# Optimization experiments

Hardware: AMD Instinct MI355X
Metric: run time of the kernel (lower is better)

The kernel has to match this reference:

```python
import jax, jax.numpy as jnp
import numpy as np

N = 100000      # nodes
E = 1600000     # edges
G = 256         # graphs in the batch
D_IN = 128
H = 128
C = 10
EPS = 1e-5      # BatchNorm eps


def setup_inputs() -> dict:
    key = jax.random.key(0)
    ks = jax.random.split(key, 32)
    inp = {
        'x': jax.random.normal(ks[0], (N, D_IN), jnp.float32),
        'edge_index': jax.random.randint(ks[1], (2, E), 0, N, dtype=jnp.int64),
        'batch': jnp.sort(jax.random.randint(ks[2], (N,), 0, G, dtype=jnp.int64)),
        'w1': jax.random.normal(ks[3], (D_IN, H), jnp.float32) * 0.05,
        'b1': jax.random.normal(ks[4], (H,), jnp.float32) * 0.05,
        'w2': jax.random.normal(ks[5], (H, H), jnp.float32) * 0.05,
        'b2': jax.random.normal(ks[6], (H,), jnp.float32) * 0.05,
        'w3': jax.random.normal(ks[7], (H, H), jnp.float32) * 0.05,
        'b3': jax.random.normal(ks[8], (H,), jnp.float32) * 0.05,
        'g1': jax.random.uniform(ks[9], (H,), jnp.float32, 0.5, 1.5),
        'be1': jax.random.normal(ks[10], (H,), jnp.float32) * 0.05,
        'm1': jax.random.normal(ks[11], (H,), jnp.float32) * 0.05,
        'v1': jax.random.uniform(ks[12], (H,), jnp.float32, 0.5, 1.5),
        'g2': jax.random.uniform(ks[13], (H,), jnp.float32, 0.5, 1.5),
        'be2': jax.random.normal(ks[14], (H,), jnp.float32) * 0.05,
        'm2': jax.random.normal(ks[15], (H,), jnp.float32) * 0.05,
        'v2': jax.random.uniform(ks[16], (H,), jnp.float32, 0.5, 1.5),
        'g3': jax.random.uniform(ks[17], (H,), jnp.float32, 0.5, 1.5),
        'be3': jax.random.normal(ks[18], (H,), jnp.float32) * 0.05,
        'm3': jax.random.normal(ks[19], (H,), jnp.float32) * 0.05,
        'v3': jax.random.uniform(ks[20], (H,), jnp.float32, 0.5, 1.5),
        'fcw1': jax.random.normal(ks[21], (H, H // 2), jnp.float32) * 0.05,
        'fcb1': jax.random.normal(ks[22], (H // 2,), jnp.float32) * 0.05,
        'fcw2': jax.random.normal(ks[23], (H // 2, C), jnp.float32) * 0.05,
        'fcb2': jax.random.normal(ks[24], (C,), jnp.float32) * 0.05,
    }
    return inp


def _gcn_norm(edge_index, n_nodes):
    # add self loops (PyG GCNConv default) and compute D^-1/2 (A+I) D^-1/2 norms
    loop = jnp.arange(n_nodes, dtype=edge_index.dtype)
    src = jnp.concatenate([edge_index[0], loop])
    dst = jnp.concatenate([edge_index[1], loop])
    deg = jax.ops.segment_sum(jnp.ones_like(dst, dtype=jnp.float32), dst, num_segments=n_nodes)
    dinv = jnp.where(deg > 0, jax.lax.rsqrt(deg), 0.0)
    norm = dinv[src] * dinv[dst]  # [E+N]
    return src, dst, norm


def _gcn_conv(x, W, b, src, dst, norm, n_nodes):
    h = x @ W                                   # [N, H]
    msg = norm[:, None] * h[src]                # gather + scale, [E+N, H]
    return jax.ops.segment_sum(msg, dst, num_segments=n_nodes) + b


def _bn_eval(x, gamma, beta, mean, var):
    return (x - mean) * jax.lax.rsqrt(var + EPS) * gamma + beta


def reference(x, edge_index, batch, w1, b1, w2, b2, w3, b3,
              g1, be1, m1, v1, g2, be2, m2, v2, g3, be3, m3, v3,
              fcw1, fcb1, fcw2, fcb2):
    n = x.shape[0]
    x = jnp.nan_to_num(x, nan=0.0, posinf=1e6, neginf=-1e6)
    src, dst, norm = _gcn_norm(edge_index, n)

    h = jax.nn.relu(_bn_eval(_gcn_conv(x, w1, b1, src, dst, norm, n), g1, be1, m1, v1))
    h = jax.nn.relu(_bn_eval(_gcn_conv(h, w2, b2, src, dst, norm, n), g2, be2, m2, v2))
    h = jax.nn.relu(_bn_eval(_gcn_conv(h, w3, b3, src, dst, norm, n), g3, be3, m3, v3))

    # global_mean_pool over graphs
    sums = jax.ops.segment_sum(h, batch, num_segments=G)            # [G, H]
    cnts = jax.ops.segment_sum(jnp.ones((n,), h.dtype), batch, num_segments=G)
    pooled = sums / jnp.maximum(cnts, 1.0)[:, None]

    out = jax.nn.relu(pooled @ fcw1 + fcb1) @ fcw2 + fcb2           # [G, C]
    return out
```

## Files before the change

### kernel.cpp

```cpp
#include <hip/hip_runtime.h>
#include <math.h>

#define NN 100000
#define EE 1600000
#define GG 256
#define HH 128
#define BSH 8
#define NBK 391
#define PASSA_WG 391
#define CAPB 5120

typedef __attribute__((ext_vector_type(8))) short short8;
typedef __attribute__((ext_vector_type(4))) float f32x4;

union U4S8 { uint4 u; short8 s; };

static __device__ __forceinline__ unsigned bf16rne(float f) {
    const unsigned u = __float_as_uint(f);
    return (u + 0x7fffu + ((u >> 16) & 1u)) >> 16;
}
static __device__ __forceinline__ unsigned packbf(float a, float b) {
    return bf16rne(a) | (bf16rne(b) << 16);
}
static __device__ __forceinline__ float bflo(unsigned u) { return __uint_as_float(u << 16); }
static __device__ __forceinline__ float bfhi(unsigned u) { return __uint_as_float(u & 0xffff0000u); }

__global__ void detect_k(const int* __restrict__ ei, const int* __restrict__ batch,
                         int* __restrict__ flags) {
    if (threadIdx.x == 0 && blockIdx.x == 0) {
        int e64 = 1;
        for (int j = 0; j < 8; ++j) {
            if (ei[2 * EE - 1 - 2 * j] != 0) { e64 = 0; break; }
        }
        flags[0] = e64;
        flags[1] = (batch[NN - 1] == 0) ? 1 : 0;
    }
}

__global__ __launch_bounds__(512) void cursinit_k(int* __restrict__ cursor) {
    const int b = blockIdx.x * 512 + threadIdx.x;
    if (b < NBK) cursor[b] = b * CAPB;
}

__global__ void bnprep_k(const float* __restrict__ b1, const float* __restrict__ g1,
                         const float* __restrict__ be1, const float* __restrict__ m1,
                         const float* __restrict__ v1,
                         const float* __restrict__ b2, const float* __restrict__ g2,
                         const float* __restrict__ be2, const float* __restrict__ m2,
                         const float* __restrict__ v2,
                         const float* __restrict__ b3, const float* __restrict__ g3,
                         const float* __restrict__ be3, const float* __restrict__ m3,
                         const float* __restrict__ v3,
                         float* __restrict__ sc, float* __restrict__ sh) {
    const int c = threadIdx.x;
    float s;
    s = g1[c] / sqrtf(v1[c] + 1e-5f);
    sc[c] = s;           sh[c] = (b1[c] - m1[c]) * s + be1[c];
    s = g2[c] / sqrtf(v2[c] + 1e-5f);
    sc[128 + c] = s;     sh[128 + c] = (b2[c] - m2[c]) * s + be2[c];
    s = g3[c] / sqrtf(v3[c] + 1e-5f);
    sc[256 + c] = s;     sh[256 + c] = (b3[c] - m3[c]) * s + be3[c];
}

__global__ __launch_bounds__(256) void wprep_k(const float* __restrict__ w1,
                                               const float* __restrict__ w2,
                                               const float* __restrict__ w3,
                                               unsigned* __restrict__ bt) {
    const int id = blockIdx.x * 256 + threadIdx.x;
    if (id >= 3 * 8192) return;
    const int w = id >> 13;
    const int rem = id & 8191;
    const int n = rem >> 6;
    const int kk = rem & 63;
    const float* W = (w == 0) ? w1 : (w == 1) ? w2 : w3;
    bt[id] = packbf(W[(2 * kk) * HH + n], W[(2 * kk + 1) * HH + n]);
}

__global__ __launch_bounds__(256) void passA_k(const int* __restrict__ ei,
                                               const int* __restrict__ flags,
                                               int* __restrict__ cursor,
                                               unsigned* __restrict__ pairs) {
    __shared__ int h[NBK];
    __shared__ int rbase[NBK];
    const int tid = threadIdx.x;
    for (int i = tid; i < NBK; i += 256) h[i] = 0;
    __syncthreads();
    const bool e64 = flags[0] != 0;
    const int base = blockIdx.x * 4096;
    int scache[16], dcache[16];
#pragma unroll
    for (int j = 0; j < 16; ++j) {
        const int e = base + j * 256 + tid;
        int s = -1, d = 0;
        if (e < EE) {
            s = e64 ? ei[2 * e] : ei[e];
            d = e64 ? ei[2 * (EE + e)] : ei[EE + e];
            atomicAdd(&h[d >> BSH], 1);
        }
        scache[j] = s; dcache[j] = d;
    }
    __syncthreads();
    for (int i = tid; i < NBK; i += 256) {
        const int c = h[i];
        rbase[i] = c ? atomicAdd(&cursor[i], c) : 0;
    }
    __syncthreads();
    for (int i = tid; i < NBK; i += 256) h[i] = 0;
    __syncthreads();
#pragma unroll
    for (int j = 0; j < 16; ++j) {
        const int s = scache[j];
        if (s >= 0) {
            const int d = dcache[j];
            const int b = d >> BSH;
            const int r = atomicAdd(&h[b], 1);
            pairs[rbase[b] + r] = ((unsigned)(d & 255) << 17) | (unsigned)s;
        }
    }
}

__global__ __launch_bounds__(256) void passB_k(const unsigned* __restrict__ pairs,
                                               const int* __restrict__ cursor,
                                               int* __restrict__ offs,
                                               int* __restrict__ degcnt,
                                               float* __restrict__ dinv,
                                               int* __restrict__ csr) {
    __shared__ unsigned pk[CAPB];
    __shared__ int cnt[256];
    __shared__ int loff[256];
    __shared__ int sc[256];
    const int tid = threadIdx.x;
    const int b = blockIdx.x;
    const int p0 = b * CAPB;
    const int np = cursor[b] - p0;
    const int nb0 = b << BSH;
    const int nnode = (NN - nb0 < 256) ? (NN - nb0) : 256;

    cnt[tid] = 0;
    __syncthreads();
    for (int i = tid; i < np; i += 256) {
        const unsigned p = pairs[p0 + i];
        pk[i] = p;
        atomicAdd(&cnt[p >> 17], 1);
    }
    __syncthreads();
    sc[tid] = cnt[tid];
    __syncthreads();
    for (int off = 1; off < 256; off <<= 1) {
        int t = (tid >= off) ? sc[tid - off] : 0;
        __syncthreads();
        sc[tid] += t;
        __syncthreads();
    }
    const int ex = sc[tid] - cnt[tid];
    loff[tid] = ex;
    if (tid < nnode) {
        const int node = nb0 + tid;
        offs[node] = p0 + ex;
        degcnt[node] = cnt[tid];
        dinv[node] = 1.0f / sqrtf((float)(cnt[tid] + 1));
    }
    __syncthreads();
    cnt[tid] = 0;
    __syncthreads();
    for (int i = tid; i < np; i += 256) {
        const unsigned p = pk[i];
        const int dl = (int)(p >> 17);
        const int r = atomicAdd(&cnt[dl], 1);
        csr[p0 + loff[dl] + r] = (int)(p & 0x1FFFFu);
    }
}

static __device__ __forceinline__ float sani(float v) {
    if (isnan(v)) return 0.0f;
    if (isinf(v)) return v > 0.0f ? 1e6f : -1e6f;
    return v;
}

template <bool AF32>
__global__ __launch_bounds__(256) void gemm_mfma_k(const float* __restrict__ Af,
                                                   const unsigned* __restrict__ Abf,
                                                   const unsigned* __restrict__ btg,
                                                   unsigned* __restrict__ C, int M) {
    __shared__ unsigned lds_u[8704];
    const int tid = threadIdx.x;
    const int wave = tid >> 6;
    const int lane = tid & 63;
    const int nl = lane & 15;
    const int q = lane >> 4;

    {
        const uint4* __restrict__ bg4 = (const uint4*)btg;
        for (int i = tid; i < 2048; i += 256) {
            const int n = i >> 4, w4 = i & 15;
            *(uint4*)&lds_u[n * 68 + w4 * 4] = bg4[n * 16 + w4];
        }
    }
    __syncthreads();

    const int row0 = blockIdx.x * 64 + wave * 16;
    const int rowa = min(row0 + nl, M - 1);

    short8 a[4];
    if (AF32) {
#pragma unroll
        for (int ks = 0; ks < 4; ++ks) {
            const float4 p = *(const float4*)(Af + (size_t)rowa * HH + ks * 32 + q * 8);
            const float4 r = *(const float4*)(Af + (size_t)rowa * HH + ks * 32 + q * 8 + 4);
            U4S8 cv;
            cv.u = make_uint4(packbf(sani(p.x), sani(p.y)), packbf(sani(p.z), sani(p.w)),
                              packbf(sani(r.x), sani(r.y)), packbf(sani(r.z), sani(r.w)));
            a[ks] = cv.s;
        }
    } else {
#pragma unroll
        for (int ks = 0; ks < 4; ++ks) {
            U4S8 cv;
            cv.u = *(const uint4*)(Abf + (size_t)rowa * 64 + ks * 16 + q * 4);
            a[ks] = cv.s;
        }
    }

    f32x4 acc[8];
#pragma unroll
    for (int t = 0; t < 8; ++t) acc[t] = (f32x4)0.0f;

    const unsigned short* __restrict__ bts = (const unsigned short*)lds_u;
#pragma unroll
    for (int ks = 0; ks < 4; ++ks) {
#pragma unroll
        for (int t = 0; t < 8; ++t) {
            const int n = t * 16 + nl;
            const short8 b = *(const short8*)(bts + n * 136 + ks * 32 + q * 8);
            acc[t] = __builtin_amdgcn_mfma_f32_16x16x32_bf16(a[ks], b, acc[t], 0, 0, 0);
        }
    }

    __syncthreads();

    float* __restrict__ cs = (float*)lds_u + wave * 16 * 132;
#pragma unroll
    for (int t = 0; t < 8; ++t) {
#pragma unroll
        for (int r = 0; r < 4; ++r) {
            cs[(q * 4 + r) * 132 + t * 16 + nl] = acc[t][r];
        }
    }
    __syncthreads();

    const int rr = lane & 15;
    const int seg = lane >> 4;
    const int rowg = row0 + rr;
    if (rowg < M) {
        const float4* crow = (const float4*)(cs + rr * 132) + seg * 8;
#pragma unroll
        for (int j = 0; j < 4; ++j) {
            const float4 fa = crow[2 * j];
            const float4 fb = crow[2 * j + 1];
            const uint4 o = make_uint4(packbf(fa.x, fa.y), packbf(fa.z, fa.w),
                                       packbf(fb.x, fb.y), packbf(fb.z, fb.w));
            *(uint4*)(C + (size_t)rowg * 64 + seg * 16 + j * 4) = o;
        }
    }
}

__global__ __launch_bounds__(256) void aggregate_k(
    const unsigned* __restrict__ hpre, const int* __restrict__ csr,
    const int* __restrict__ offs, const int* __restrict__ cnt,
    const float* __restrict__ dinv,
    const float* __restrict__ bnsc, const float* __restrict__ bnsh,
    unsigned* __restrict__ xout) {
    const int v = __builtin_amdgcn_readfirstlane(blockIdx.x * 4 + (threadIdx.x >> 6));
    const int lane = threadIdx.x & 63;
    const int cg = lane & 15;
    const int sub = lane >> 4;
    const int c8 = cg * 8;

    const float dv = dinv[v];
    const int start = offs[v];
    const int n = cnt[v];
    const char* __restrict__ hb = (const char*)hpre;
    const unsigned cgo = (unsigned)(cg << 4);

    float acc[8];
#pragma unroll
    for (int j = 0; j < 8; ++j) acc[j] = 0.0f;

    for (int i = 0; i < n; i += 16) {
        const int e0 = i + sub, e1 = i + 4 + sub, e2 = i + 8 + sub, e3 = i + 12 + sub;
        const int nm1 = n - 1;
        const int s0 = csr[start + min(e0, nm1)];
        const int s1 = csr[start + min(e1, nm1)];
        const int s2 = csr[start + min(e2, nm1)];
        const int s3 = csr[start + min(e3, nm1)];
        const float w0 = (e0 < n) ? dinv[s0] : 0.0f;
        const float w1 = (e1 < n) ? dinv[s1] : 0.0f;
        const float w2 = (e2 < n) ? dinv[s2] : 0.0f;
        const float w3 = (e3 < n) ? dinv[s3] : 0.0f;
        const uint4 r0 = *(const uint4*)(hb + (((unsigned)s0 << 8) | cgo));
        const uint4 r1 = *(const uint4*)(hb + (((unsigned)s1 << 8) | cgo));
        const uint4 r2 = *(const uint4*)(hb + (((unsigned)s2 << 8) | cgo));
        const uint4 r3 = *(const uint4*)(hb + (((unsigned)s3 << 8) | cgo));

        acc[0] += w0 * bflo(r0.x); acc[1] += w0 * bfhi(r0.x);
        acc[2] += w0 * bflo(r0.y); acc[3] += w0 * bfhi(r0.y);
        acc[4] += w0 * bflo(r0.z); acc[5] += w0 * bfhi(r0.z);
        acc[6] += w0 * bflo(r0.w); acc[7] += w0 * bfhi(r0.w);
        acc[0] += w1 * bflo(r1.x); acc[1] += w1 * bfhi(r1.x);
        acc[2] += w1 * bflo(r1.y); acc[3] += w1 * bfhi(r1.y);
        acc[4] += w1 * bflo(r1.z); acc[5] += w1 * bfhi(r1.z);
        acc[6] += w1 * bflo(r1.w); acc[7] += w1 * bfhi(r1.w);
        acc[0] += w2 * bflo(r2.x); acc[1] += w2 * bfhi(r2.x);
        acc[2] += w2 * bflo(r2.y); acc[3] += w2 * bfhi(r2.y);
        acc[4] += w2 * bflo(r2.z); acc[5] += w2 * bfhi(r2.z);
        acc[6] += w2 * bflo(r2.w); acc[7] += w2 * bfhi(r2.w);
        acc[0] += w3 * bflo(r3.x); acc[1] += w3 * bfhi(r3.x);
        acc[2] += w3 * bflo(r3.y); acc[3] += w3 * bfhi(r3.y);
        acc[4] += w3 * bflo(r3.z); acc[5] += w3 * bfhi(r3.z);
        acc[6] += w3 * bflo(r3.w); acc[7] += w3 * bfhi(r3.w);
    }

#pragma unroll
    for (int j = 0; j < 8; ++j) {
        acc[j] += __shfl_xor(acc[j], 16);
        acc[j] += __shfl_xor(acc[j], 32);
    }

    if (sub == 0) {
        const float4 sca = *(const float4*)(bnsc + c8);
        const float4 scb = *(const float4*)(bnsc + c8 + 4);
        const float4 sha = *(const float4*)(bnsh + c8);
        const float4 shb = *(const float4*)(bnsh + c8 + 4);
        const uint4 rs = *(const uint4*)(hb + (((unsigned)v << 8) | cgo));
        const float dv2 = dv * dv;
        const float s0 = dv * acc[0] + dv2 * bflo(rs.x);
        const float s1 = dv * acc[1] + dv2 * bfhi(rs.x);
        const float s2 = dv * acc[2] + dv2 * bflo(rs.y);
        const float s3 = dv * acc[3] + dv2 * bfhi(rs.y);
        const float s4 = dv * acc[4] + dv2 * bflo(rs.z);
        const float s5 = dv * acc[5] + dv2 * bfhi(rs.z);
        const float s6 = dv * acc[6] + dv2 * bflo(rs.w);
        const float s7 = dv * acc[7] + dv2 * bfhi(rs.w);
        const float y0 = fmaxf(s0 * sca.x + sha.x, 0.0f);
        const float y1 = fmaxf(s1 * sca.y + sha.y, 0.0f);
        const float y2 = fmaxf(s2 * sca.z + sha.z, 0.0f);
        const float y3 = fmaxf(s3 * sca.w + sha.w, 0.0f);
        const float y4 = fmaxf(s4 * scb.x + shb.x, 0.0f);
        const float y5 = fmaxf(s5 * scb.y + shb.y, 0.0f);
        const float y6 = fmaxf(s6 * scb.z + shb.z, 0.0f);
        const float y7 = fmaxf(s7 * scb.w + shb.w, 0.0f);
        *(uint4*)(xout + (size_t)v * 64 + cg * 4) =
            make_uint4(packbf(y0, y1), packbf(y2, y3), packbf(y4, y5), packbf(y6, y7));
    }
}

__global__ __launch_bounds__(256) void pool_sum_k(
    const unsigned* __restrict__ x, const int* __restrict__ batch,
    const int* __restrict__ flags, float* __restrict__ psum,
    int* __restrict__ gcnt) {
    const int wave = threadIdx.x >> 6;
    const int lane = threadIdx.x & 63;
    const int row0 = blockIdx.x * 64 + wave * 16;
    if (row0 >= NN) return;
    const bool b64 = flags[1] != 0;

    float sx = 0.0f, sy = 0.0f;
    int cur = -1, runlen = 0;
#pragma unroll
    for (int r = 0; r < 16; ++r) {
        const int row = row0 + r;
        if (row >= NN) break;
        const int g = b64 ? batch[2 * row] : batch[row];
        if (g != cur) {
            if (cur >= 0) {
                atomicAdd(&psum[cur * HH + lane * 2 + 0], sx);
                atomicAdd(&psum[cur * HH + lane * 2 + 1], sy);
                if (lane == 0) atomicAdd(&gcnt[cur], runlen);
            }
            cur = g; sx = 0.0f; sy = 0.0f; runlen = 0;
        }
        const unsigned u = x[(size_t)row * 64 + lane];
        sx += bflo(u);
        sy += bfhi(u);
        ++runlen;
    }
    if (cur >= 0) {
        atomicAdd(&psum[cur * HH + lane * 2 + 0], sx);
        atomicAdd(&psum[cur * HH + lane * 2 + 1], sy);
        if (lane == 0) atomicAdd(&gcnt[cur], runlen);
    }
}

__global__ __launch_bounds__(128) void head_k(
    const float* __restrict__ psum, const int* __restrict__ gcnt,
    const float* __restrict__ fw1, const float* __restrict__ fb1,
    const float* __restrict__ fw2, const float* __restrict__ fb2,
    float* __restrict__ out) {
    __shared__ float pooled[128];
    __shared__ float hid[64];
    const int g = blockIdx.x;
    const int tid = threadIdx.x;

    const int cntn = gcnt[g];
    pooled[tid] = psum[g * HH + tid] / (float)(cntn > 0 ? cntn : 1);
    __syncthreads();

    if (tid < 64) {
        float a = fb1[tid];
#pragma unroll 4
        for (int k = 0; k < 128; ++k) a += pooled[k] * fw1[k * 64 + tid];
        hid[tid] = fmaxf(a, 0.0f);
    }
    __syncthreads();
    if (tid < 10) {
        float a = fb2[tid];
#pragma unroll
        for (int k = 0; k < 64; ++k) a += hid[k] * fw2[k * 10 + tid];
        out[g * 10 + tid] = a;
    }
}

extern "C" void kernel_launch(void* const* d_in, const int* in_sizes, int n_in,
                              void* d_out, int out_size, void* d_ws, size_t ws_size,
                              hipStream_t stream) {
    const float* x_in  = (const float*)d_in[0];
    const int*   ei    = (const int*)d_in[1];
    const int*   batch = (const int*)d_in[2];
    const float* w1 = (const float*)d_in[3];
    const float* b1 = (const float*)d_in[4];
    const float* w2 = (const float*)d_in[5];
    const float* b2 = (const float*)d_in[6];
    const float* w3 = (const float*)d_in[7];
    const float* b3 = (const float*)d_in[8];
    const float* g1 = (const float*)d_in[9];
    const float* be1 = (const float*)d_in[10];
    const float* m1 = (const float*)d_in[11];
    const float* v1 = (const float*)d_in[12];
    const float* g2 = (const float*)d_in[13];
    const float* be2 = (const float*)d_in[14];
    const float* m2 = (const float*)d_in[15];
    const float* v2 = (const float*)d_in[16];
    const float* g3 = (const float*)d_in[17];
    const float* be3 = (const float*)d_in[18];
    const float* m3 = (const float*)d_in[19];
    const float* v3 = (const float*)d_in[20];
    const float* fw1 = (const float*)d_in[21];
    const float* fb1 = (const float*)d_in[22];
    const float* fw2 = (const float*)d_in[23];
    const float* fb2 = (const float*)d_in[24];
    float* out = (float*)d_out;

    size_t off = 0;
    char* base = (char*)d_ws;
    auto alloc = [&](size_t bytes) -> void* {
        void* p = base + off;
        off += (bytes + 255) & ~(size_t)255;
        return p;
    };
    int*      degcnt = (int*)alloc((size_t)NN * 4);
    float*    dinv   = (float*)alloc((size_t)NN * 4);
    int*      offs   = (int*)alloc((size_t)NN * 4);
    int*      cursor = (int*)alloc((size_t)NBK * 4);
    int*      flags  = (int*)alloc(256);
    float*    bnsc   = (float*)alloc(3 * 128 * 4);
    float*    bnsh   = (float*)alloc(3 * 128 * 4);
    unsigned* btg    = (unsigned*)alloc(3 * 8192 * 4);
    float*    psum   = (float*)alloc((size_t)GG * HH * 4);
    int*      gcnt   = (int*)alloc((size_t)GG * 4);
    int*      csr    = (int*)alloc((size_t)NBK * CAPB * 4);
    unsigned* pairs  = (unsigned*)alloc((size_t)NBK * CAPB * 4);
    unsigned* bufx   = (unsigned*)alloc((size_t)NN * 64 * 4);
    unsigned* hpre   = (unsigned*)alloc((size_t)NN * 64 * 4);
    if (off > ws_size) return;

    detect_k<<<1, 64, 0, stream>>>(ei, batch, flags);
    cursinit_k<<<1, 512, 0, stream>>>(cursor);
    bnprep_k<<<1, 128, 0, stream>>>(b1, g1, be1, m1, v1,
                                    b2, g2, be2, m2, v2,
                                    b3, g3, be3, m3, v3, bnsc, bnsh);
    wprep_k<<<96, 256, 0, stream>>>(w1, w2, w3, btg);
    hipMemsetAsync(psum, 0, (size_t)GG * HH * 4, stream);
    hipMemsetAsync(gcnt, 0, (size_t)GG * 4, stream);
    passA_k<<<PASSA_WG, 256, 0, stream>>>(ei, flags, cursor, pairs);
    passB_k<<<NBK, 256, 0, stream>>>(pairs, cursor, offs, degcnt, dinv, csr);

    const int ggrid = (NN + 63) / 64;
    const int agrid = NN / 4;

    gemm_mfma_k<true><<<ggrid, 256, 0, stream>>>(x_in, nullptr, btg, hpre, NN);
    aggregate_k<<<agrid, 256, 0, stream>>>(hpre, csr, offs, degcnt, dinv,
                                           bnsc, bnsh, bufx);
    gemm_mfma_k<false><<<ggrid, 256, 0, stream>>>(nullptr, bufx, btg + 8192, hpre, NN);
    aggregate_k<<<agrid, 256, 0, stream>>>(hpre, csr, offs, degcnt, dinv,
                                           bnsc + 128, bnsh + 128, bufx);
    gemm_mfma_k<false><<<ggrid, 256, 0, stream>>>(nullptr, bufx, btg + 16384, hpre, NN);
    aggregate_k<<<agrid, 256, 0, stream>>>(hpre, csr, offs, degcnt, dinv,
                                           bnsc + 256, bnsh + 256, bufx);

    pool_sum_k<<<ggrid, 256, 0, stream>>>(bufx, batch, flags, psum, gcnt);
    head_k<<<GG, 128, 0, stream>>>(psum, gcnt, fw1, fb1, fw2, fb2, out);
}
```

Baseline: 470.1 us.

## Prescale GEMM output by source dinv and pad CSR rows with self-loop and zero row

```diff
diff --git a/kernel.cpp b/kernel.cpp
--- a/kernel.cpp
+++ b/kernel.cpp
@@ -8,7 +8,7 @@
 #define BSH 8
 #define NBK 391
 #define PASSA_WG 391
-#define CAPB 5120
+#define CAPB 5632
 
 typedef __attribute__((ext_vector_type(8))) short short8;
 typedef __attribute__((ext_vector_type(4))) float f32x4;
@@ -144,7 +144,9 @@
         atomicAdd(&cnt[p >> 17], 1);
     }
     __syncthreads();
-    sc[tid] = cnt[tid];
+    const int creal = cnt[tid];
+    const int cpad = (tid < nnode) ? ((creal + 4) & ~3) : 0;
+    sc[tid] = cpad;
     __syncthreads();
     for (int off = 1; off < 256; off <<= 1) {
         int t = (tid >= off) ? sc[tid - off] : 0;
@@ -152,13 +154,13 @@
         sc[tid] += t;
         __syncthreads();
     }
-    const int ex = sc[tid] - cnt[tid];
+    const int ex = sc[tid] - cpad;
     loff[tid] = ex;
     if (tid < nnode) {
         const int node = nb0 + tid;
         offs[node] = p0 + ex;
-        degcnt[node] = cnt[tid];
-        dinv[node] = 1.0f / sqrtf((float)(cnt[tid] + 1));
+        degcnt[node] = creal;
+        dinv[node] = 1.0f / sqrtf((float)(creal + 1));
     }
     __syncthreads();
     cnt[tid] = 0;
@@ -169,6 +171,11 @@
         const int r = atomicAdd(&cnt[dl], 1);
         csr[p0 + loff[dl] + r] = (int)(p & 0x1FFFFu);
     }
+    if (tid < nnode) {
+        const int basep = p0 + loff[tid];
+        csr[basep + creal] = nb0 + tid;
+        for (int j = creal + 1; j < cpad; ++j) csr[basep + j] = NN;
+    }
 }
 
 static __device__ __forceinline__ float sani(float v) {
@@ -181,6 +188,7 @@
 __global__ __launch_bounds__(256) void gemm_mfma_k(const float* __restrict__ Af,
                                                    const unsigned* __restrict__ Abf,
                                                    const unsigned* __restrict__ btg,
+                                                   const float* __restrict__ dinv,
                                                    unsigned* __restrict__ C, int M) {
     __shared__ unsigned lds_u[8704];
     const int tid = threadIdx.x;
@@ -252,15 +260,23 @@
     const int seg = lane >> 4;
     const int rowg = row0 + rr;
     if (rowg < M) {
+        const float dsc = dinv[rowg];
         const float4* crow = (const float4*)(cs + rr * 132) + seg * 8;
 #pragma unroll
         for (int j = 0; j < 4; ++j) {
             const float4 fa = crow[2 * j];
             const float4 fb = crow[2 * j + 1];
-            const uint4 o = make_uint4(packbf(fa.x, fa.y), packbf(fa.z, fa.w),
-                                       packbf(fb.x, fb.y), packbf(fb.z, fb.w));
+            const uint4 o = make_uint4(packbf(dsc * fa.x, dsc * fa.y),
+                                       packbf(dsc * fa.z, dsc * fa.w),
+                                       packbf(dsc * fb.x, dsc * fb.y),
+                                       packbf(dsc * fb.z, dsc * fb.w));
             *(uint4*)(C + (size_t)rowg * 64 + seg * 16 + j * 4) = o;
         }
+    } else if (rowg == M) {
+        const uint4 z = make_uint4(0, 0, 0, 0);
+#pragma unroll
+        for (int j = 0; j < 4; ++j)
+            *(uint4*)(C + (size_t)M * 64 + seg * 16 + j * 4) = z;
     }
 }
 
@@ -278,7 +294,7 @@
 
     const float dv = dinv[v];
     const int start = offs[v];
-    const int n = cnt[v];
+    const int npad = (cnt[v] + 4) & ~3;
     const char* __restrict__ hb = (const char*)hpre;
     const unsigned cgo = (unsigned)(cg << 4);
 
@@ -286,38 +302,28 @@
 #pragma unroll
     for (int j = 0; j < 8; ++j) acc[j] = 0.0f;
 
-    for (int i = 0; i < n; i += 16) {
-        const int e0 = i + sub, e1 = i + 4 + sub, e2 = i + 8 + sub, e3 = i + 12 + sub;
-        const int nm1 = n - 1;
-        const int s0 = csr[start + min(e0, nm1)];
-        const int s1 = csr[start + min(e1, nm1)];
-        const int s2 = csr[start + min(e2, nm1)];
-        const int s3 = csr[start + min(e3, nm1)];
-        const float w0 = (e0 < n) ? dinv[s0] : 0.0f;
-        const float w1 = (e1 < n) ? dinv[s1] : 0.0f;
-        const float w2 = (e2 < n) ? dinv[s2] : 0.0f;
-        const float w3 = (e3 < n) ? dinv[s3] : 0.0f;
-        const uint4 r0 = *(const uint4*)(hb + (((unsigned)s0 << 8) | cgo));
-        const uint4 r1 = *(const uint4*)(hb + (((unsigned)s1 << 8) | cgo));
-        const uint4 r2 = *(const uint4*)(hb + (((unsigned)s2 << 8) | cgo));
-        const uint4 r3 = *(const uint4*)(hb + (((unsigned)s3 << 8) | cgo));
-
-        acc[0] += w0 * bflo(r0.x); acc[1] += w0 * bfhi(r0.x);
-        acc[2] += w0 * bflo(r0.y); acc[3] += w0 * bfhi(r0.y);
-        acc[4] += w0 * bflo(r0.z); acc[5] += w0 * bfhi(r0.z);
-        acc[6] += w0 * bflo(r0.w); acc[7] += w0 * bfhi(r0.w);
-        acc[0] += w1 * bflo(r1.x); acc[1] += w1 * bfhi(r1.x);
-        acc[2] += w1 * bflo(r1.y); acc[3] += w1 * bfhi(r1.y);
-        acc[4] += w1 * bflo(r1.z); acc[5] += w1 * bfhi(r1.z);
-        acc[6] += w1 * bflo(r1.w); acc[7] += w1 * bfhi(r1.w);
-        acc[0] += w2 * bflo(r2.x); acc[1] += w2 * bfhi(r2.x);
-        acc[2] += w2 * bflo(r2.y); acc[3] += w2 * bfhi(r2.y);
-        acc[4] += w2 * bflo(r2.z); acc[5] += w2 * bfhi(r2.z);
-        acc[6] += w2 * bflo(r2.w); acc[7] += w2 * bfhi(r2.w);
-        acc[0] += w3 * bflo(r3.x); acc[1] += w3 * bfhi(r3.x);
-        acc[2] += w3 * bflo(r3.y); acc[3] += w3 * bfhi(r3.y);
-        acc[4] += w3 * bflo(r3.z); acc[5] += w3 * bfhi(r3.z);
-        acc[6] += w3 * bflo(r3.w); acc[7] += w3 * bfhi(r3.w);
+    int i = 0;
+    for (; i + 8 <= npad; i += 8) {
+        const int sA = csr[start + i + sub];
+        const int sB = csr[start + i + 4 + sub];
+        const uint4 rA = *(const uint4*)(hb + (((unsigned)sA << 8) | cgo));
+        const uint4 rB = *(const uint4*)(hb + (((unsigned)sB << 8) | cgo));
+        acc[0] += bflo(rA.x) + bflo(rB.x);
+        acc[1] += bfhi(rA.x) + bfhi(rB.x);
+        acc[2] += bflo(rA.y) + bflo(rB.y);
+        acc[3] += bfhi(rA.y) + bfhi(rB.y);
+        acc[4] += bflo(rA.z) + bflo(rB.z);
+        acc[5] += bfhi(rA.z) + bfhi(rB.z);
+        acc[6] += bflo(rA.w) + bflo(rB.w);
+        acc[7] += bfhi(rA.w) + bfhi(rB.w);
+    }
+    if (i < npad) {
+        const int s = csr[start + i + sub];
+        const uint4 r = *(const uint4*)(hb + (((unsigned)s << 8) | cgo));
+        acc[0] += bflo(r.x); acc[1] += bfhi(r.x);
+        acc[2] += bflo(r.y); acc[3] += bfhi(r.y);
+        acc[4] += bflo(r.z); acc[5] += bfhi(r.z);
+        acc[6] += bflo(r.w); acc[7] += bfhi(r.w);
     }
 
 #pragma unroll
@@ -331,24 +337,14 @@
         const float4 scb = *(const float4*)(bnsc + c8 + 4);
         const float4 sha = *(const float4*)(bnsh + c8);
         const float4 shb = *(const float4*)(bnsh + c8 + 4);
-        const uint4 rs = *(const uint4*)(hb + (((unsigned)v << 8) | cgo));
-        const float dv2 = dv * dv;
-        const float s0 = dv * acc[0] + dv2 * bflo(rs.x);
-        const float s1 = dv * acc[1] + dv2 * bfhi(rs.x);
-        const float s2 = dv * acc[2] + dv2 * bflo(rs.y);
-        const float s3 = dv * acc[3] + dv2 * bfhi(rs.y);
-        const float s4 = dv * acc[4] + dv2 * bflo(rs.z);
-        const float s5 = dv * acc[5] + dv2 * bfhi(rs.z);
-        const float s6 = dv * acc[6] + dv2 * bflo(rs.w);
-        const float s7 = dv * acc[7] + dv2 * bfhi(rs.w);
-        const float y0 = fmaxf(s0 * sca.x + sha.x, 0.0f);
-        const float y1 = fmaxf(s1 * sca.y + sha.y, 0.0f);
-        const float y2 = fmaxf(s2 * sca.z + sha.z, 0.0f);
-        const float y3 = fmaxf(s3 * sca.w + sha.w, 0.0f);
-        const float y4 = fmaxf(s4 * scb.x + shb.x, 0.0f);
-        const float y5 = fmaxf(s5 * scb.y + shb.y, 0.0f);
-        const float y6 = fmaxf(s6 * scb.z + shb.z, 0.0f);
-        const float y7 = fmaxf(s7 * scb.w + shb.w, 0.0f);
+        const float y0 = fmaxf(dv * acc[0] * sca.x + sha.x, 0.0f);
+        const float y1 = fmaxf(dv * acc[1] * sca.y + sha.y, 0.0f);
+        const float y2 = fmaxf(dv * acc[2] * sca.z + sha.z, 0.0f);
+        const float y3 = fmaxf(dv * acc[3] * sca.w + sha.w, 0.0f);
+        const float y4 = fmaxf(dv * acc[4] * scb.x + shb.x, 0.0f);
+        const float y5 = fmaxf(dv * acc[5] * scb.y + shb.y, 0.0f);
+        const float y6 = fmaxf(dv * acc[6] * scb.z + shb.z, 0.0f);
+        const float y7 = fmaxf(dv * acc[7] * scb.w + shb.w, 0.0f);
         *(uint4*)(xout + (size_t)v * 64 + cg * 4) =
             make_uint4(packbf(y0, y1), packbf(y2, y3), packbf(y4, y5), packbf(y6, y7));
     }
@@ -470,7 +466,7 @@
     int*      csr    = (int*)alloc((size_t)NBK * CAPB * 4);
     unsigned* pairs  = (unsigned*)alloc((size_t)NBK * CAPB * 4);
     unsigned* bufx   = (unsigned*)alloc((size_t)NN * 64 * 4);
-    unsigned* hpre   = (unsigned*)alloc((size_t)NN * 64 * 4);
+    unsigned* hpre   = (unsigned*)alloc((size_t)(NN + 1) * 64 * 4);
     if (off > ws_size) return;
 
     detect_k<<<1, 64, 0, stream>>>(ei, batch, flags);
@@ -487,13 +483,13 @@
     const int ggrid = (NN + 63) / 64;
     const int agrid = NN / 4;
 
-    gemm_mfma_k<true><<<ggrid, 256, 0, stream>>>(x_in, nullptr, btg, hpre, NN);
+    gemm_mfma_k<true><<<ggrid, 256, 0, stream>>>(x_in, nullptr, btg, dinv, hpre, NN);
     aggregate_k<<<agrid, 256, 0, stream>>>(hpre, csr, offs, degcnt, dinv,
                                            bnsc, bnsh, bufx);
-    gemm_mfma_k<false><<<ggrid, 256, 0, stream>>>(nullptr, bufx, btg + 8192, hpre, NN);
+    gemm_mfma_k<false><<<ggrid, 256, 0, stream>>>(nullptr, bufx, btg + 8192, dinv, hpre, NN);
     aggregate_k<<<agrid, 256, 0, stream>>>(hpre, csr, offs, degcnt, dinv,
                                            bnsc + 128, bnsh + 128, bufx);
-    gemm_mfma_k<false><<<ggrid, 256, 0, stream>>>(nullptr, bufx, btg + 16384, hpre, NN);
+    gemm_mfma_k<false><<<ggrid, 256, 0, stream>>>(nullptr, bufx, btg + 16384, dinv, hpre, NN);
     aggregate_k<<<agrid, 256, 0, stream>>>(hpre, csr, offs, degcnt, dinv,
                                            bnsc + 256, bnsh + 256, bufx);
 
```

Result: faster. 456.5 us (-2.9%).
